# Optimization experiments

Hardware: AMD Instinct MI355X
Metric: run time of the kernel (lower is better)

The kernel has to match this reference:

```python
import jax, jax.numpy as jnp
import numpy as np

BETA = 0.95
THR = 1.0
NUM_STEPS = 100
ALPHA = 2.0  # snntorch atan surrogate default

@jax.custom_vjp
def atan_spike(x):
    return (x > 0).astype(x.dtype)

def _as_fwd(x):
    return (x > 0).astype(x.dtype), x

def _as_bwd(x, g):
    return (g * (ALPHA / 2) / (1 + (jnp.pi / 2 * ALPHA * x) ** 2),)

atan_spike.defvjp(_as_fwd, _as_bwd)


def setup_inputs() -> dict:
    key = jax.random.key(0)
    ks = jax.random.split(key, 9)
    B = 16384
    SH, NH, CO, OUT = 1024, 1024, 256, 64
    s = 0.05
    return {
        "x": jax.random.normal(ks[0], (B, 105), jnp.float32),
        "snn_w1": jax.random.normal(ks[1], (SH, 5), jnp.float32) * s,
        "snn_b1": jnp.zeros((SH,), jnp.float32),
        "snn_w2": jax.random.normal(ks[2], (OUT, SH), jnp.float32) * s,
        "snn_b2": jnp.zeros((OUT,), jnp.float32),
        "nn_w1": jax.random.normal(ks[3], (NH, 5), jnp.float32) * s,
        "nn_b1": jnp.zeros((NH,), jnp.float32),
        "nn_w2": jax.random.normal(ks[4], (OUT, NH), jnp.float32) * s,
        "nn_b2": jnp.zeros((OUT,), jnp.float32),
        "conv_w": jax.random.normal(ks[5], (32, 1, 3), jnp.float32) * s,
        "conv_b": jnp.zeros((32,), jnp.float32),
        "cnn_fc_w": jax.random.normal(ks[6], (CO, 32 * 50), jnp.float32) * s,
        "cnn_fc_b": jnp.zeros((CO,), jnp.float32),
        "comb_w": jax.random.normal(ks[7], (OUT, 2 * OUT + CO), jnp.float32) * s,
        "comb_b": jnp.zeros((OUT,), jnp.float32),
    }


def _forward(x, snn_w1, snn_b1, snn_w2, snn_b2, nn_w1, nn_b1, nn_w2, nn_b2,
             conv_w, conv_b, cnn_fc_w, cnn_fc_b, comb_w, comb_b):
    feats = x[:, :5]                 # [B,5]
    wave = x[:, 5:][:, None, :]      # [B,1,100]
    B = x.shape[0]

    # ---- SNN branch (LIF, beta leak, subtract reset, threshold 1.0) ----
    cur1 = feats @ snn_w1.T + snn_b1  # input current is constant across steps

    def step(carry, _):
        mem1, spk1, mem2, spk2 = carry
        # reset term uses detached spike (snntorch mem_reset detaches)
        mem1 = BETA * mem1 + cur1 - jax.lax.stop_gradient(spk1) * THR
        spk1 = atan_spike(mem1 - THR)
        cur2 = spk1 @ snn_w2.T + snn_b2
        mem2 = BETA * mem2 + cur2 - jax.lax.stop_gradient(spk2) * THR
        spk2 = atan_spike(mem2 - THR)
        return (mem1, spk1, mem2, spk2), spk2

    z1 = jnp.zeros_like(cur1)
    z2 = jnp.zeros((B, snn_w2.shape[0]), cur1.dtype)
    _, spk_rec = jax.lax.scan(step, (z1, z1, z2, z2), None, length=NUM_STEPS)
    snn_out = spk_rec.mean(axis=0)   # [B,OUT]

    # ---- MLP branch ----
    nn_out = jax.nn.relu(feats @ nn_w1.T + nn_b1) @ nn_w2.T + nn_b2

    # ---- CNN branch ----
    c = jax.lax.conv_general_dilated(wave, conv_w, (1,), [(1, 1)],
                                     dimension_numbers=("NCW", "OIW", "NCW"))
    c = jax.nn.relu(c + conv_b[None, :, None])   # [B,32,100]
    c = c.reshape(B, 32, 50, 2).max(axis=-1)      # MaxPool1d(k=2,s=2)
    cnn_out = c.reshape(B, -1) @ cnn_fc_w.T + cnn_fc_b

    combined = jnp.concatenate([snn_out, nn_out, cnn_out], axis=1)
    return combined @ comb_w.T + comb_b


def reference(x, snn_w1, snn_b1, snn_w2, snn_b2, nn_w1, nn_b1, nn_w2, nn_b2,
              conv_w, conv_b, cnn_fc_w, cnn_fc_b, comb_w, comb_b):
    return _forward(x, snn_w1, snn_b1, snn_w2, snn_b2, nn_w1, nn_b1, nn_w2,
                    nn_b2, conv_w, conv_b, cnn_fc_w, cnn_fc_b, comb_w, comb_b)
```

## Files before the change

### kernel.cpp

```cpp
#include <hip/hip_runtime.h>

typedef __bf16 bf16x8_t __attribute__((ext_vector_type(8)));
typedef float f32x4_t __attribute__((ext_vector_type(4)));
typedef float f32x2_t __attribute__((ext_vector_type(2)));

#define NSTEPS 100
#define PB0 0u
#define PB1 32768u
#define COMBF 51200u

static __device__ __forceinline__ unsigned short f2bfu(float v) {
  union { __bf16 h; unsigned short u; } c; c.h = (__bf16)v; return c.u;
}
static __device__ __forceinline__ unsigned int pack2bf(float a, float b) {
  return (unsigned)f2bfu(a) | ((unsigned)f2bfu(b) << 16);
}
static __device__ __forceinline__ float asf(unsigned u) {
  union { unsigned u; float f; } c; c.u = u; return c.f;
}
static __device__ __forceinline__ unsigned asu(float f) {
  union { float f; unsigned u; } c; c.f = f; return c.u;
}
union BF8U { unsigned int u[4]; bf16x8_t v; };

static __device__ __forceinline__ bf16x8_t bfrag_f32(const float* __restrict__ p, float s) {
  BF8U r;
#pragma unroll
  for (int i = 0; i < 4; ++i) r.u[i] = pack2bf(p[2*i]*s, p[2*i+1]*s);
  return r.v;
}

static __device__ __forceinline__ void comb_store(unsigned char* ldsp, int k, int row, float v) {
  *(unsigned short*)(ldsp + COMBF +
      (unsigned)((k >> 5)*1024 + (((k >> 3) & 3)*16 + row)*16 + (k & 7)*2)) = f2bfu(v);
}

__global__ __launch_bounds__(512, 2)
void hybrid_v5(const float* __restrict__ x,
               const float* __restrict__ snn_w1, const float* __restrict__ snn_b1,
               const float* __restrict__ snn_w2, const float* __restrict__ snn_b2,
               const float* __restrict__ nn_w1,  const float* __restrict__ nn_b1,
               const float* __restrict__ nn_w2,  const float* __restrict__ nn_b2,
               const float* __restrict__ conv_w, const float* __restrict__ conv_b,
               const float* __restrict__ fc_w,   const float* __restrict__ fc_b,
               const float* __restrict__ comb_w, const float* __restrict__ comb_b,
               const unsigned short* __restrict__ fcwb, int use_bf,
               float* __restrict__ out)
{
  __shared__ __align__(16) unsigned char lds[65536];
  const int tid  = threadIdx.x;
  const int w    = tid >> 6;
  const int l    = tid & 63;
  const int q    = l >> 4;
  const int m    = l & 15;
  const int row0 = blockIdx.x * 16;

  const int hi  = w >> 2;
  const int ntr = w & 3;
  const int rn  = ntr*16 + m;
  const int rA  = hi*4 + q;
  const int rB  = rA + 8;

  const float* xr = x + (row0 + m)*105;
  const float f0 = xr[0], f1 = xr[1], f2 = xr[2], f3 = xr[3], f4 = xr[4];
  const float b2l = snn_b2[rn];

  bf16x8_t bfr[4][4];
#pragma unroll
  for (int ci = 0; ci < 4; ++ci)
#pragma unroll
    for (int nt = 0; nt < 4; ++nt)
      bfr[ci][nt] = bfrag_f32(snn_w2 + (nt*16 + m)*1024 + (w*4 + ci)*32 + q*8, 1.f);

  f32x2_t cb[16], mb[16];
  {
    const int kb = w*128 + q*8;
#pragma unroll
    for (int ci = 0; ci < 4; ++ci) {
      const float* wp = snn_w1 + (kb + ci*32)*5;
      float wa[40];
#pragma unroll
      for (int u2 = 0; u2 < 10; ++u2) {
        const float4 t4 = *(const float4*)(wp + u2*4);
        wa[u2*4+0] = t4.x; wa[u2*4+1] = t4.y; wa[u2*4+2] = t4.z; wa[u2*4+3] = t4.w;
      }
      float cc[8];
#pragma unroll
      for (int j = 0; j < 8; ++j)
        cc[j] = f0*wa[j*5] + f1*wa[j*5+1] + f2*wa[j*5+2] + f3*wa[j*5+3] + f4*wa[j*5+4]
              + snn_b1[kb + ci*32 + j];
#pragma unroll
      for (int jj = 0; jj < 4; ++jj) {
        cb[ci*4+jj].x = cc[2*jj];   cb[ci*4+jj].y = cc[2*jj+1];
        mb[ci*4+jj].x = 0.f;        mb[ci*4+jj].y = 0.f;
      }
    }
  }

  BF8U afr[4];
#pragma unroll
  for (int ci = 0; ci < 4; ++ci)
#pragma unroll
    for (int jj = 0; jj < 4; ++jj) afr[ci].u[jj] = 0u;

  auto lif_step = [&]() {
#pragma clang fp contract(off)
#pragma unroll
    for (int ci = 0; ci < 4; ++ci) {
#pragma unroll
      for (int jj = 0; jj < 4; ++jj) {
        const int idx = ci*4 + jj;
        const unsigned u = afr[ci].u[jj];
        f32x2_t sp;
        sp.x = asf(u << 16);
        sp.y = asf(u & 0xFFFF0000u);
        f32x2_t mm = mb[idx];
        mm = mm * 0.95f;
        mm = mm + cb[idx];
        mm = mm - sp;
        mb[idx] = mm;
        const float t0 = mm.x > 1.f ? 1.f : 0.f;
        const float t1 = mm.y > 1.f ? 1.f : 0.f;
        afr[ci].u[jj] = __builtin_amdgcn_perm(asu(t1), asu(t0), 0x07060302u);
      }
    }
  };
  lif_step();

  float m2A = 0.f, s2A = 0.f, cntA = 0.f;
  float m2B = 0.f, s2B = 0.f, cntB = 0.f;

  const unsigned pbase  = (unsigned)(ntr*1024 + hi*256 + m*16 + q*4);
  const unsigned wtbase = (unsigned)((w*4*64 + l)*16);
  const f32x4_t z4 = {0.f, 0.f, 0.f, 0.f};

  auto phase = [&](unsigned cur, unsigned prv, bool doRead, bool doLif) {
    float vA[8], vB[8];
    if (doRead) {
#pragma unroll
      for (int s = 0; s < 8; ++s) vA[s] = *(const float*)(lds + prv + pbase + (unsigned)(s*4096));
#pragma unroll
      for (int s = 0; s < 8; ++s) vB[s] = *(const float*)(lds + prv + pbase + 512u + (unsigned)(s*4096));
    }
    f32x4_t acc[4] = {z4, z4, z4, z4};
#pragma unroll
    for (int ci = 0; ci < 4; ++ci)
#pragma unroll
      for (int nt = 0; nt < 4; ++nt)
        acc[nt] = __builtin_amdgcn_mfma_f32_16x16x32_bf16(afr[ci].v, bfr[ci][nt], acc[nt], 0,0,0);
#pragma unroll
    for (int nt = 0; nt < 4; ++nt)
      *(f32x4_t*)(lds + cur + wtbase + (unsigned)(nt*1024)) = acc[nt];
    if (doLif) lif_step();
    if (doRead) {
      float curA = (((vA[0]+vA[1]) + (vA[2]+vA[3])) + ((vA[4]+vA[5]) + (vA[6]+vA[7]))) + b2l;
      float curB = (((vB[0]+vB[1]) + (vB[2]+vB[3])) + ((vB[4]+vB[5]) + (vB[6]+vB[7]))) + b2l;
      m2A = __fsub_rn(__fadd_rn(__fmul_rn(0.95f, m2A), curA), s2A);
      s2A = m2A > 1.f ? 1.f : 0.f;  cntA += s2A;
      m2B = __fsub_rn(__fadd_rn(__fmul_rn(0.95f, m2B), curB), s2B);
      s2B = m2B > 1.f ? 1.f : 0.f;  cntB += s2B;
    }
    __syncthreads();
  };

#pragma unroll 1
  for (int tt = 0; tt < NSTEPS; tt += 2) {
    phase(PB0, PB1, tt > 0, true);
    phase(PB1, PB0, true,  tt + 1 < NSTEPS - 1);
  }

#pragma unroll
  for (int ci = 0; ci < 4; ++ci)
#pragma unroll
    for (int nt = 0; nt < 4; ++nt)
      bfr[ci][nt] = bfrag_f32(nn_w2 + (nt*16 + m)*1024 + (w*4 + ci)*32 + q*8, 1.f);
  {
    float vA[8], vB[8];
#pragma unroll
    for (int s = 0; s < 8; ++s) vA[s] = *(const float*)(lds + PB1 + pbase + (unsigned)(s*4096));
#pragma unroll
    for (int s = 0; s < 8; ++s) vB[s] = *(const float*)(lds + PB1 + pbase + 512u + (unsigned)(s*4096));
    float curA = (((vA[0]+vA[1]) + (vA[2]+vA[3])) + ((vA[4]+vA[5]) + (vA[6]+vA[7]))) + b2l;
    float curB = (((vB[0]+vB[1]) + (vB[2]+vB[3])) + ((vB[4]+vB[5]) + (vB[6]+vB[7]))) + b2l;
    m2A = __fsub_rn(__fadd_rn(__fmul_rn(0.95f, m2A), curA), s2A);
    s2A = m2A > 1.f ? 1.f : 0.f;  cntA += s2A;
    m2B = __fsub_rn(__fadd_rn(__fmul_rn(0.95f, m2B), curB), s2B);
    s2B = m2B > 1.f ? 1.f : 0.f;  cntB += s2B;

    BF8U hfr[4];
    const int kb = w*128 + q*8;
#pragma unroll
    for (int ci = 0; ci < 4; ++ci) {
      const float* wp = nn_w1 + (kb + ci*32)*5;
      float wa[40];
#pragma unroll
      for (int u2 = 0; u2 < 10; ++u2) {
        const float4 t4 = *(const float4*)(wp + u2*4);
        wa[u2*4+0] = t4.x; wa[u2*4+1] = t4.y; wa[u2*4+2] = t4.z; wa[u2*4+3] = t4.w;
      }
      float hv[8];
#pragma unroll
      for (int j = 0; j < 8; ++j) {
        const float h = f0*wa[j*5] + f1*wa[j*5+1] + f2*wa[j*5+2] + f3*wa[j*5+3] + f4*wa[j*5+4]
                      + nn_b1[kb + ci*32 + j];
        hv[j] = fmaxf(h, 0.f);
      }
#pragma unroll
      for (int jj = 0; jj < 4; ++jj) hfr[ci].u[jj] = pack2bf(hv[2*jj], hv[2*jj+1]);
    }
    f32x4_t acc[4] = {z4, z4, z4, z4};
#pragma unroll
    for (int ci = 0; ci < 4; ++ci)
#pragma unroll
      for (int nt = 0; nt < 4; ++nt)
        acc[nt] = __builtin_amdgcn_mfma_f32_16x16x32_bf16(hfr[ci].v, bfr[ci][nt], acc[nt], 0,0,0);
#pragma unroll
    for (int nt = 0; nt < 4; ++nt)
      *(f32x4_t*)(lds + PB0 + wtbase + (unsigned)(nt*1024)) = acc[nt];
  }
  __syncthreads();
  {
    float vA[8], vB[8];
#pragma unroll
    for (int s = 0; s < 8; ++s) vA[s] = *(const float*)(lds + PB0 + pbase + (unsigned)(s*4096));
#pragma unroll
    for (int s = 0; s < 8; ++s) vB[s] = *(const float*)(lds + PB0 + pbase + 512u + (unsigned)(s*4096));
    const float nA = (((vA[0]+vA[1]) + (vA[2]+vA[3])) + ((vA[4]+vA[5]) + (vA[6]+vA[7]))) + nn_b2[rn];
    const float nB = (((vB[0]+vB[1]) + (vB[2]+vB[3])) + ((vB[4]+vB[5]) + (vB[6]+vB[7]))) + nn_b2[rn];
    comb_store(lds, rn,      rA, cntA * 0.0078125f);
    comb_store(lds, rn,      rB, cntB * 0.0078125f);
    comb_store(lds, 64 + rn, rA, nA);
    comb_store(lds, 64 + rn, rB, nB);
  }
  __syncthreads();

  {
    const int ch = tid >> 4;
    const float cw0 = conv_w[ch*3+0], cw1 = conv_w[ch*3+1], cw2 = conv_w[ch*3+2];
    const float cbb = conv_b[ch];
    const float* xw = xr + 5;
    float xm1 = 0.f, x0v = xw[0];
#pragma unroll 1
    for (int p = 0; p < 50; ++p) {
      const float xp1 = xw[2*p + 1];
      const float xp2 = (p < 49) ? xw[2*p + 2] : 0.f;
      const float av = cw0*xm1 + cw1*x0v + cw2*xp1 + cbb;
      const float bv = cw0*x0v + cw1*xp1 + cw2*xp2 + cbb;
      const float pv = fmaxf(fmaxf(av, 0.f), fmaxf(bv, 0.f));
      const int k = ch*50 + p;
      *(unsigned short*)(lds + (unsigned)((k>>5)*1024 + (((k>>3)&3)*16 + m)*16 + (k&7)*2)) = f2bfu(pv);
      xm1 = xp1; x0v = xp2;
    }
  }
  __syncthreads();

  {
    const int c0 = (w*2 + 0)*16 + m;
    const int c1 = (w*2 + 1)*16 + m;
    f32x4_t e0 = z4, o0 = z4, e1 = z4, o1 = z4;
    if (use_bf) {
#pragma unroll 2
      for (int kc = 0; kc < 50; kc += 2) {
        const bf16x8_t a0 = *(const bf16x8_t*)(lds + (unsigned)((kc*64 + l)*16));
        const bf16x8_t a1 = *(const bf16x8_t*)(lds + (unsigned)(((kc+1)*64 + l)*16));
        e0 = __builtin_amdgcn_mfma_f32_16x16x32_bf16(a0, *(const bf16x8_t*)(fcwb + c0*1600 + kc*32 + q*8), e0, 0,0,0);
        o0 = __builtin_amdgcn_mfma_f32_16x16x32_bf16(a1, *(const bf16x8_t*)(fcwb + c0*1600 + (kc+1)*32 + q*8), o0, 0,0,0);
        e1 = __builtin_amdgcn_mfma_f32_16x16x32_bf16(a0, *(const bf16x8_t*)(fcwb + c1*1600 + kc*32 + q*8), e1, 0,0,0);
        o1 = __builtin_amdgcn_mfma_f32_16x16x32_bf16(a1, *(const bf16x8_t*)(fcwb + c1*1600 + (kc+1)*32 + q*8), o1, 0,0,0);
      }
    } else {
#pragma unroll 2
      for (int kc = 0; kc < 50; kc += 2) {
        const bf16x8_t a0 = *(const bf16x8_t*)(lds + (unsigned)((kc*64 + l)*16));
        const bf16x8_t a1 = *(const bf16x8_t*)(lds + (unsigned)(((kc+1)*64 + l)*16));
        e0 = __builtin_amdgcn_mfma_f32_16x16x32_bf16(a0, bfrag_f32(fc_w + c0*1600 + kc*32 + q*8, 1.f), e0, 0,0,0);
        o0 = __builtin_amdgcn_mfma_f32_16x16x32_bf16(a1, bfrag_f32(fc_w + c0*1600 + (kc+1)*32 + q*8, 1.f), o0, 0,0,0);
        e1 = __builtin_amdgcn_mfma_f32_16x16x32_bf16(a0, bfrag_f32(fc_w + c1*1600 + kc*32 + q*8, 1.f), e1, 0,0,0);
        o1 = __builtin_amdgcn_mfma_f32_16x16x32_bf16(a1, bfrag_f32(fc_w + c1*1600 + (kc+1)*32 + q*8, 1.f), o1, 0,0,0);
      }
    }
    const float fb0 = fc_b[c0], fb1 = fc_b[c1];
#pragma unroll
    for (int r = 0; r < 4; ++r) {
      comb_store(lds, 128 + c0, q*4 + r, (e0[r] + o0[r]) + fb0);
      comb_store(lds, 128 + c1, q*4 + r, (e1[r] + o1[r]) + fb1);
    }
  }
  __syncthreads();

  if (w < 4) {
    const int cn = w*16 + m;
    f32x4_t oe = z4, oo = z4;
#pragma unroll
    for (int kc = 0; kc < 12; kc += 2) {
      const bf16x8_t a0 = *(const bf16x8_t*)(lds + COMBF + (unsigned)((kc*64 + l)*16));
      const bf16x8_t a1 = *(const bf16x8_t*)(lds + COMBF + (unsigned)(((kc+1)*64 + l)*16));
      const float s0 = (kc    < 2) ? 1.28f : 1.f;
      const float s1 = (kc+1 < 2) ? 1.28f : 1.f;
      oe = __builtin_amdgcn_mfma_f32_16x16x32_bf16(a0, bfrag_f32(comb_w + cn*384 + kc*32 + q*8, s0), oe, 0,0,0);
      oo = __builtin_amdgcn_mfma_f32_16x16x32_bf16(a1, bfrag_f32(comb_w + cn*384 + (kc+1)*32 + q*8, s1), oo, 0,0,0);
    }
    const float cb2 = comb_b[cn];
#pragma unroll
    for (int r = 0; r < 4; ++r)
      out[(row0 + q*4 + r)*64 + cn] = (oe[r] + oo[r]) + cb2;
  }
}

__global__ __launch_bounds__(256)
void fcw_to_bf16(const float* __restrict__ src, unsigned short* __restrict__ dst) {
  const int i = (blockIdx.x * 256 + threadIdx.x) * 4;
  const float4 v = *(const float4*)(src + i);
  ushort4 o;
  o.x = f2bfu(v.x); o.y = f2bfu(v.y); o.z = f2bfu(v.z); o.w = f2bfu(v.w);
  *(ushort4*)(dst + i) = o;
}

extern "C" void kernel_launch(void* const* d_in, const int* in_sizes, int n_in,
                              void* d_out, int out_size, void* d_ws, size_t ws_size,
                              hipStream_t stream) {
  const float* x       = (const float*)d_in[0];
  const float* snn_w1  = (const float*)d_in[1];
  const float* snn_b1  = (const float*)d_in[2];
  const float* snn_w2  = (const float*)d_in[3];
  const float* snn_b2  = (const float*)d_in[4];
  const float* nn_w1   = (const float*)d_in[5];
  const float* nn_b1   = (const float*)d_in[6];
  const float* nn_w2   = (const float*)d_in[7];
  const float* nn_b2   = (const float*)d_in[8];
  const float* conv_w  = (const float*)d_in[9];
  const float* conv_b  = (const float*)d_in[10];
  const float* fc_w    = (const float*)d_in[11];
  const float* fc_b    = (const float*)d_in[12];
  const float* comb_w  = (const float*)d_in[13];
  const float* comb_b  = (const float*)d_in[14];
  float* outp = (float*)d_out;

  const int rows = in_sizes[0] / 105;
  const int grid = rows / 16;

  const size_t fcw_elems = (size_t)in_sizes[11];
  const int use_bf = (ws_size >= fcw_elems * 2) ? 1 : 0;
  unsigned short* fcwb = (unsigned short*)d_ws;
  if (use_bf) {
    fcw_to_bf16<<<dim3((unsigned)(fcw_elems / 1024)), dim3(256), 0, stream>>>(fc_w, fcwb);
  }

  hybrid_v5<<<dim3(grid), dim3(512), 0, stream>>>(
      x, snn_w1, snn_b1, snn_w2, snn_b2,
      nn_w1, nn_b1, nn_w2, nn_b2,
      conv_w, conv_b, fc_w, fc_b, comb_w, comb_b,
      fcwb, use_bf, outp);
}
```

Measured before the change: 766.5 us.

## Halve block to four waves with wider per-wave K slice in SNN loop

Launches 256-thread blocks instead of 512, giving each wave twice as many hidden neurons (8 K-chunks) in the recurrent SNN step and the MLP/CNN stages. This cuts the cross-wave LDS partial-sum reduction from 8 to 4 partials per step and makes the barrier cover fewer waves. In exchange, per-wave register use roughly doubles (weights and membrane state held in VGPRs) and fewer waves are resident to hide latency, while each wave issues twice as many serial MFMAs per step. The LIF update also switches from packed float2 math to scalar rn intrinsics.

Result: slower. 820.0 us (+7.0%).

```diff
diff --git a/kernel.cpp b/kernel.cpp
--- a/kernel.cpp
+++ b/kernel.cpp
@@ -2,11 +2,10 @@
 
 typedef __bf16 bf16x8_t __attribute__((ext_vector_type(8)));
 typedef float f32x4_t __attribute__((ext_vector_type(4)));
-typedef float f32x2_t __attribute__((ext_vector_type(2)));
 
 #define NSTEPS 100
 #define PB0 0u
-#define PB1 32768u
+#define PB1 16384u
 #define COMBF 51200u
 
 static __device__ __forceinline__ unsigned short f2bfu(float v) {
@@ -35,8 +34,8 @@
       (unsigned)((k >> 5)*1024 + (((k >> 3) & 3)*16 + row)*16 + (k & 7)*2)) = f2bfu(v);
 }
 
-__global__ __launch_bounds__(512, 2)
-void hybrid_v5(const float* __restrict__ x,
+__global__ __launch_bounds__(256, 1)
+void hybrid_v8(const float* __restrict__ x,
                const float* __restrict__ snn_w1, const float* __restrict__ snn_b1,
                const float* __restrict__ snn_w2, const float* __restrict__ snn_b2,
                const float* __restrict__ nn_w1,  const float* __restrict__ nn_b1,
@@ -55,28 +54,24 @@
   const int m    = l & 15;
   const int row0 = blockIdx.x * 16;
 
-  const int hi  = w >> 2;
-  const int ntr = w & 3;
-  const int rn  = ntr*16 + m;
-  const int rA  = hi*4 + q;
-  const int rB  = rA + 8;
+  const int rcol = w*16 + m;
 
   const float* xr = x + (row0 + m)*105;
   const float f0 = xr[0], f1 = xr[1], f2 = xr[2], f3 = xr[3], f4 = xr[4];
-  const float b2l = snn_b2[rn];
-
-  bf16x8_t bfr[4][4];
-#pragma unroll
-  for (int ci = 0; ci < 4; ++ci)
+  const float b2l = snn_b2[rcol];
+
+  bf16x8_t bfr[8][4];
+#pragma unroll
+  for (int ci = 0; ci < 8; ++ci)
 #pragma unroll
     for (int nt = 0; nt < 4; ++nt)
-      bfr[ci][nt] = bfrag_f32(snn_w2 + (nt*16 + m)*1024 + (w*4 + ci)*32 + q*8, 1.f);
-
-  f32x2_t cb[16], mb[16];
-  {
-    const int kb = w*128 + q*8;
-#pragma unroll
-    for (int ci = 0; ci < 4; ++ci) {
+      bfr[ci][nt] = bfrag_f32(snn_w2 + (nt*16 + m)*1024 + (w*8 + ci)*32 + q*8, 1.f);
+
+  float c[64], mem[64];
+  {
+    const int kb = w*256 + q*8;
+#pragma unroll
+    for (int ci = 0; ci < 8; ++ci) {
       const float* wp = snn_w1 + (kb + ci*32)*5;
       float wa[40];
 #pragma unroll
@@ -84,67 +79,58 @@
         const float4 t4 = *(const float4*)(wp + u2*4);
         wa[u2*4+0] = t4.x; wa[u2*4+1] = t4.y; wa[u2*4+2] = t4.z; wa[u2*4+3] = t4.w;
       }
-      float cc[8];
-#pragma unroll
-      for (int j = 0; j < 8; ++j)
-        cc[j] = f0*wa[j*5] + f1*wa[j*5+1] + f2*wa[j*5+2] + f3*wa[j*5+3] + f4*wa[j*5+4]
-              + snn_b1[kb + ci*32 + j];
+#pragma unroll
+      for (int j = 0; j < 8; ++j) {
+        c[ci*8+j] = f0*wa[j*5] + f1*wa[j*5+1] + f2*wa[j*5+2] + f3*wa[j*5+3] + f4*wa[j*5+4]
+                  + snn_b1[kb + ci*32 + j];
+        mem[ci*8+j] = 0.f;
+      }
+    }
+  }
+
+  BF8U afr[8];
+#pragma unroll
+  for (int ci = 0; ci < 8; ++ci)
+#pragma unroll
+    for (int jj = 0; jj < 4; ++jj) afr[ci].u[jj] = 0u;
+
+  auto lif_step = [&]() {
+#pragma unroll
+    for (int ci = 0; ci < 8; ++ci) {
 #pragma unroll
       for (int jj = 0; jj < 4; ++jj) {
-        cb[ci*4+jj].x = cc[2*jj];   cb[ci*4+jj].y = cc[2*jj+1];
-        mb[ci*4+jj].x = 0.f;        mb[ci*4+jj].y = 0.f;
-      }
-    }
-  }
-
-  BF8U afr[4];
-#pragma unroll
-  for (int ci = 0; ci < 4; ++ci)
-#pragma unroll
-    for (int jj = 0; jj < 4; ++jj) afr[ci].u[jj] = 0u;
-
-  auto lif_step = [&]() {
-#pragma clang fp contract(off)
-#pragma unroll
-    for (int ci = 0; ci < 4; ++ci) {
-#pragma unroll
-      for (int jj = 0; jj < 4; ++jj) {
-        const int idx = ci*4 + jj;
+        const int i0 = ci*8 + 2*jj;
         const unsigned u = afr[ci].u[jj];
-        f32x2_t sp;
-        sp.x = asf(u << 16);
-        sp.y = asf(u & 0xFFFF0000u);
-        f32x2_t mm = mb[idx];
-        mm = mm * 0.95f;
-        mm = mm + cb[idx];
-        mm = mm - sp;
-        mb[idx] = mm;
-        const float t0 = mm.x > 1.f ? 1.f : 0.f;
-        const float t1 = mm.y > 1.f ? 1.f : 0.f;
+        const float sp0 = asf(u << 16);
+        const float sp1 = asf(u & 0xFFFF0000u);
+        mem[i0]   = __fsub_rn(__fadd_rn(__fmul_rn(0.95f, mem[i0]),   c[i0]),   sp0);
+        mem[i0+1] = __fsub_rn(__fadd_rn(__fmul_rn(0.95f, mem[i0+1]), c[i0+1]), sp1);
+        const float t0 = mem[i0]   > 1.f ? 1.f : 0.f;
+        const float t1 = mem[i0+1] > 1.f ? 1.f : 0.f;
         afr[ci].u[jj] = __builtin_amdgcn_perm(asu(t1), asu(t0), 0x07060302u);
       }
     }
   };
   lif_step();
 
-  float m2A = 0.f, s2A = 0.f, cntA = 0.f;
-  float m2B = 0.f, s2B = 0.f, cntB = 0.f;
-
-  const unsigned pbase  = (unsigned)(ntr*1024 + hi*256 + m*16 + q*4);
-  const unsigned wtbase = (unsigned)((w*4*64 + l)*16);
+  float m2[4] = {0.f,0.f,0.f,0.f}, s2[4] = {0.f,0.f,0.f,0.f}, cnt[4] = {0.f,0.f,0.f,0.f};
+
+  const unsigned wtbase = (unsigned)(w*4096 + l*16);
+  const unsigned rbase  = (unsigned)(w*1024 + (l&15)*16 + (l>>4)*4);
   const f32x4_t z4 = {0.f, 0.f, 0.f, 0.f};
 
   auto phase = [&](unsigned cur, unsigned prv, bool doRead, bool doLif) {
-    float vA[8], vB[8];
+    float v[16];
     if (doRead) {
 #pragma unroll
-      for (int s = 0; s < 8; ++s) vA[s] = *(const float*)(lds + prv + pbase + (unsigned)(s*4096));
-#pragma unroll
-      for (int s = 0; s < 8; ++s) vB[s] = *(const float*)(lds + prv + pbase + 512u + (unsigned)(s*4096));
+      for (int s = 0; s < 4; ++s)
+#pragma unroll
+        for (int i = 0; i < 4; ++i)
+          v[s*4+i] = *(const float*)(lds + prv + rbase + (unsigned)(s*4096 + i*256));
     }
     f32x4_t acc[4] = {z4, z4, z4, z4};
 #pragma unroll
-    for (int ci = 0; ci < 4; ++ci)
+    for (int ci = 0; ci < 8; ++ci)
 #pragma unroll
       for (int nt = 0; nt < 4; ++nt)
         acc[nt] = __builtin_amdgcn_mfma_f32_16x16x32_bf16(afr[ci].v, bfr[ci][nt], acc[nt], 0,0,0);
@@ -153,12 +139,12 @@
       *(f32x4_t*)(lds + cur + wtbase + (unsigned)(nt*1024)) = acc[nt];
     if (doLif) lif_step();
     if (doRead) {
-      float curA = (((vA[0]+vA[1]) + (vA[2]+vA[3])) + ((vA[4]+vA[5]) + (vA[6]+vA[7]))) + b2l;
-      float curB = (((vB[0]+vB[1]) + (vB[2]+vB[3])) + ((vB[4]+vB[5]) + (vB[6]+vB[7]))) + b2l;
-      m2A = __fsub_rn(__fadd_rn(__fmul_rn(0.95f, m2A), curA), s2A);
-      s2A = m2A > 1.f ? 1.f : 0.f;  cntA += s2A;
-      m2B = __fsub_rn(__fadd_rn(__fmul_rn(0.95f, m2B), curB), s2B);
-      s2B = m2B > 1.f ? 1.f : 0.f;  cntB += s2B;
+#pragma unroll
+      for (int i = 0; i < 4; ++i) {
+        const float cc = ((v[0+i] + v[4+i]) + (v[8+i] + v[12+i])) + b2l;
+        m2[i] = __fsub_rn(__fadd_rn(__fmul_rn(0.95f, m2[i]), cc), s2[i]);
+        s2[i] = m2[i] > 1.f ? 1.f : 0.f;  cnt[i] += s2[i];
+      }
     }
     __syncthreads();
   };
@@ -170,27 +156,28 @@
   }
 
 #pragma unroll
-  for (int ci = 0; ci < 4; ++ci)
+  for (int ci = 0; ci < 8; ++ci)
 #pragma unroll
     for (int nt = 0; nt < 4; ++nt)
-      bfr[ci][nt] = bfrag_f32(nn_w2 + (nt*16 + m)*1024 + (w*4 + ci)*32 + q*8, 1.f);
-  {
-    float vA[8], vB[8];
-#pragma unroll
-    for (int s = 0; s < 8; ++s) vA[s] = *(const float*)(lds + PB1 + pbase + (unsigned)(s*4096));
-#pragma unroll
-    for (int s = 0; s < 8; ++s) vB[s] = *(const float*)(lds + PB1 + pbase + 512u + (unsigned)(s*4096));
-    float curA = (((vA[0]+vA[1]) + (vA[2]+vA[3])) + ((vA[4]+vA[5]) + (vA[6]+vA[7]))) + b2l;
-    float curB = (((vB[0]+vB[1]) + (vB[2]+vB[3])) + ((vB[4]+vB[5]) + (vB[6]+vB[7]))) + b2l;
-    m2A = __fsub_rn(__fadd_rn(__fmul_rn(0.95f, m2A), curA), s2A);
-    s2A = m2A > 1.f ? 1.f : 0.f;  cntA += s2A;
-    m2B = __fsub_rn(__fadd_rn(__fmul_rn(0.95f, m2B), curB), s2B);
-    s2B = m2B > 1.f ? 1.f : 0.f;  cntB += s2B;
-
-    BF8U hfr[4];
-    const int kb = w*128 + q*8;
-#pragma unroll
-    for (int ci = 0; ci < 4; ++ci) {
+      bfr[ci][nt] = bfrag_f32(nn_w2 + (nt*16 + m)*1024 + (w*8 + ci)*32 + q*8, 1.f);
+  {
+    float v[16];
+#pragma unroll
+    for (int s = 0; s < 4; ++s)
+#pragma unroll
+      for (int i = 0; i < 4; ++i)
+        v[s*4+i] = *(const float*)(lds + PB1 + rbase + (unsigned)(s*4096 + i*256));
+#pragma unroll
+    for (int i = 0; i < 4; ++i) {
+      const float cc = ((v[0+i] + v[4+i]) + (v[8+i] + v[12+i])) + b2l;
+      m2[i] = __fsub_rn(__fadd_rn(__fmul_rn(0.95f, m2[i]), cc), s2[i]);
+      s2[i] = m2[i] > 1.f ? 1.f : 0.f;  cnt[i] += s2[i];
+    }
+
+    BF8U hfr[8];
+    const int kb = w*256 + q*8;
+#pragma unroll
+    for (int ci = 0; ci < 8; ++ci) {
       const float* wp = nn_w1 + (kb + ci*32)*5;
       float wa[40];
 #pragma unroll
@@ -210,7 +197,7 @@
     }
     f32x4_t acc[4] = {z4, z4, z4, z4};
 #pragma unroll
-    for (int ci = 0; ci < 4; ++ci)
+    for (int ci = 0; ci < 8; ++ci)
 #pragma unroll
       for (int nt = 0; nt < 4; ++nt)
         acc[nt] = __builtin_amdgcn_mfma_f32_16x16x32_bf16(hfr[ci].v, bfr[ci][nt], acc[nt], 0,0,0);
@@ -220,75 +207,87 @@
   }
   __syncthreads();
   {
-    float vA[8], vB[8];
-#pragma unroll
-    for (int s = 0; s < 8; ++s) vA[s] = *(const float*)(lds + PB0 + pbase + (unsigned)(s*4096));
-#pragma unroll
-    for (int s = 0; s < 8; ++s) vB[s] = *(const float*)(lds + PB0 + pbase + 512u + (unsigned)(s*4096));
-    const float nA = (((vA[0]+vA[1]) + (vA[2]+vA[3])) + ((vA[4]+vA[5]) + (vA[6]+vA[7]))) + nn_b2[rn];
-    const float nB = (((vB[0]+vB[1]) + (vB[2]+vB[3])) + ((vB[4]+vB[5]) + (vB[6]+vB[7]))) + nn_b2[rn];
-    comb_store(lds, rn,      rA, cntA * 0.0078125f);
-    comb_store(lds, rn,      rB, cntB * 0.0078125f);
-    comb_store(lds, 64 + rn, rA, nA);
-    comb_store(lds, 64 + rn, rB, nB);
+    float v[16];
+#pragma unroll
+    for (int s = 0; s < 4; ++s)
+#pragma unroll
+      for (int i = 0; i < 4; ++i)
+        v[s*4+i] = *(const float*)(lds + PB0 + rbase + (unsigned)(s*4096 + i*256));
+#pragma unroll
+    for (int i = 0; i < 4; ++i) {
+      const float nv = ((v[0+i] + v[4+i]) + (v[8+i] + v[12+i])) + nn_b2[rcol];
+      comb_store(lds, rcol,      i*4 + q, cnt[i] * 0.0078125f);
+      comb_store(lds, 64 + rcol, i*4 + q, nv);
+    }
   }
   __syncthreads();
 
   {
     const int ch = tid >> 4;
-    const float cw0 = conv_w[ch*3+0], cw1 = conv_w[ch*3+1], cw2 = conv_w[ch*3+2];
-    const float cbb = conv_b[ch];
+    const float a0w = conv_w[ch*3+0], a1w = conv_w[ch*3+1], a2w = conv_w[ch*3+2];
+    const float b0w = conv_w[(ch+16)*3+0], b1w = conv_w[(ch+16)*3+1], b2w = conv_w[(ch+16)*3+2];
+    const float cba = conv_b[ch], cbb = conv_b[ch+16];
     const float* xw = xr + 5;
     float xm1 = 0.f, x0v = xw[0];
 #pragma unroll 1
     for (int p = 0; p < 50; ++p) {
       const float xp1 = xw[2*p + 1];
       const float xp2 = (p < 49) ? xw[2*p + 2] : 0.f;
-      const float av = cw0*xm1 + cw1*x0v + cw2*xp1 + cbb;
-      const float bv = cw0*x0v + cw1*xp1 + cw2*xp2 + cbb;
-      const float pv = fmaxf(fmaxf(av, 0.f), fmaxf(bv, 0.f));
-      const int k = ch*50 + p;
-      *(unsigned short*)(lds + (unsigned)((k>>5)*1024 + (((k>>3)&3)*16 + m)*16 + (k&7)*2)) = f2bfu(pv);
+      const float aa = a0w*xm1 + a1w*x0v + a2w*xp1 + cba;
+      const float ab = a0w*x0v + a1w*xp1 + a2w*xp2 + cba;
+      const float pa = fmaxf(fmaxf(aa, 0.f), fmaxf(ab, 0.f));
+      const float ba = b0w*xm1 + b1w*x0v + b2w*xp1 + cbb;
+      const float bb = b0w*x0v + b1w*xp1 + b2w*xp2 + cbb;
+      const float pb = fmaxf(fmaxf(ba, 0.f), fmaxf(bb, 0.f));
+      const int ka = ch*50 + p;
+      const int kb2 = (ch+16)*50 + p;
+      *(unsigned short*)(lds + (unsigned)((ka>>5)*1024 + (((ka>>3)&3)*16 + m)*16 + (ka&7)*2)) = f2bfu(pa);
+      *(unsigned short*)(lds + (unsigned)((kb2>>5)*1024 + (((kb2>>3)&3)*16 + m)*16 + (kb2&7)*2)) = f2bfu(pb);
       xm1 = xp1; x0v = xp2;
     }
   }
   __syncthreads();
 
   {
-    const int c0 = (w*2 + 0)*16 + m;
-    const int c1 = (w*2 + 1)*16 + m;
-    f32x4_t e0 = z4, o0 = z4, e1 = z4, o1 = z4;
+    f32x4_t fe[4] = {z4, z4, z4, z4};
+    f32x4_t fo[4] = {z4, z4, z4, z4};
     if (use_bf) {
 #pragma unroll 2
       for (int kc = 0; kc < 50; kc += 2) {
         const bf16x8_t a0 = *(const bf16x8_t*)(lds + (unsigned)((kc*64 + l)*16));
         const bf16x8_t a1 = *(const bf16x8_t*)(lds + (unsigned)(((kc+1)*64 + l)*16));
-        e0 = __builtin_amdgcn_mfma_f32_16x16x32_bf16(a0, *(const bf16x8_t*)(fcwb + c0*1600 + kc*32 + q*8), e0, 0,0,0);
-        o0 = __builtin_amdgcn_mfma_f32_16x16x32_bf16(a1, *(const bf16x8_t*)(fcwb + c0*1600 + (kc+1)*32 + q*8), o0, 0,0,0);
-        e1 = __builtin_amdgcn_mfma_f32_16x16x32_bf16(a0, *(const bf16x8_t*)(fcwb + c1*1600 + kc*32 + q*8), e1, 0,0,0);
-        o1 = __builtin_amdgcn_mfma_f32_16x16x32_bf16(a1, *(const bf16x8_t*)(fcwb + c1*1600 + (kc+1)*32 + q*8), o1, 0,0,0);
+#pragma unroll
+        for (int nt = 0; nt < 4; ++nt) {
+          const int cn = w*64 + nt*16 + m;
+          fe[nt] = __builtin_amdgcn_mfma_f32_16x16x32_bf16(a0, *(const bf16x8_t*)(fcwb + cn*1600 + kc*32 + q*8), fe[nt], 0,0,0);
+          fo[nt] = __builtin_amdgcn_mfma_f32_16x16x32_bf16(a1, *(const bf16x8_t*)(fcwb + cn*1600 + (kc+1)*32 + q*8), fo[nt], 0,0,0);
+        }
       }
     } else {
 #pragma unroll 2
       for (int kc = 0; kc < 50; kc += 2) {
         const bf16x8_t a0 = *(const bf16x8_t*)(lds + (unsigned)((kc*64 + l)*16));
         const bf16x8_t a1 = *(const bf16x8_t*)(lds + (unsigned)(((kc+1)*64 + l)*16));
-        e0 = __builtin_amdgcn_mfma_f32_16x16x32_bf16(a0, bfrag_f32(fc_w + c0*1600 + kc*32 + q*8, 1.f), e0, 0,0,0);
-        o0 = __builtin_amdgcn_mfma_f32_16x16x32_bf16(a1, bfrag_f32(fc_w + c0*1600 + (kc+1)*32 + q*8, 1.f), o0, 0,0,0);
-        e1 = __builtin_amdgcn_mfma_f32_16x16x32_bf16(a0, bfrag_f32(fc_w + c1*1600 + kc*32 + q*8, 1.f), e1, 0,0,0);
-        o1 = __builtin_amdgcn_mfma_f32_16x16x32_bf16(a1, bfrag_f32(fc_w + c1*1600 + (kc+1)*32 + q*8, 1.f), o1, 0,0,0);
-      }
-    }
-    const float fb0 = fc_b[c0], fb1 = fc_b[c1];
-#pragma unroll
-    for (int r = 0; r < 4; ++r) {
-      comb_store(lds, 128 + c0, q*4 + r, (e0[r] + o0[r]) + fb0);
-      comb_store(lds, 128 + c1, q*4 + r, (e1[r] + o1[r]) + fb1);
+#pragma unroll
+        for (int nt = 0; nt < 4; ++nt) {
+          const int cn = w*64 + nt*16 + m;
+          fe[nt] = __builtin_amdgcn_mfma_f32_16x16x32_bf16(a0, bfrag_f32(fc_w + cn*1600 + kc*32 + q*8, 1.f), fe[nt], 0,0,0);
+          fo[nt] = __builtin_amdgcn_mfma_f32_16x16x32_bf16(a1, bfrag_f32(fc_w + cn*1600 + (kc+1)*32 + q*8, 1.f), fo[nt], 0,0,0);
+        }
+      }
+    }
+#pragma unroll
+    for (int nt = 0; nt < 4; ++nt) {
+      const int cn = w*64 + nt*16 + m;
+      const float fb = fc_b[cn];
+#pragma unroll
+      for (int r = 0; r < 4; ++r)
+        comb_store(lds, 128 + cn, q*4 + r, (fe[nt][r] + fo[nt][r]) + fb);
     }
   }
   __syncthreads();
 
-  if (w < 4) {
+  {
     const int cn = w*16 + m;
     f32x4_t oe = z4, oo = z4;
 #pragma unroll
@@ -346,7 +345,7 @@
     fcw_to_bf16<<<dim3((unsigned)(fcw_elems / 1024)), dim3(256), 0, stream>>>(fc_w, fcwb);
   }
 
-  hybrid_v5<<<dim3(grid), dim3(512), 0, stream>>>(
+  hybrid_v8<<<dim3(grid), dim3(256), 0, stream>>>(
       x, snn_w1, snn_b1, snn_w2, snn_b2,
       nn_w1, nn_b1, nn_w2, nn_b2,
       conv_w, conv_b, fc_w, fc_b, comb_w, comb_b,
```

## Specialize warps into LIF producers and MFMA consumers with LDS spike exchange

Applied to the files above, without the earlier changes.

Splits the 8 waves into two roles. Four waves run the layer-1 LIF update over 256 neurons each and write bf16 spike fragments to double-buffered LDS. The other four waves hold the snn_w2 fragments for their K slice, run the MFMAs, reduce partial sums through LDS and update the layer-2 LIF. The goal is to overlap the elementwise LIF work with the matrix work across steps and to cut the per-wave partial-sum reduction from 8 ways to 4. The cost is higher register use per wave, since each producer wave keeps 32 state pairs and each consumer wave keeps 32 weight fragments. LDS grows to 96 KB of dynamic shared memory, which may lower occupancy below the 2 blocks per CU requested in launch_bounds.

Measured after the change: 779.7 us. Within noise of the previous version (+1.7%).

```diff
diff --git a/kernel.cpp b/kernel.cpp
--- a/kernel.cpp
+++ b/kernel.cpp
@@ -5,9 +5,11 @@
 typedef float f32x2_t __attribute__((ext_vector_type(2)));
 
 #define NSTEPS 100
-#define PB0 0u
-#define PB1 32768u
-#define COMBF 51200u
+#define SB0 0u
+#define SB1 32768u
+#define PBU0 65536u
+#define PBU1 81920u
+#define COMBF 86016u
 
 static __device__ __forceinline__ unsigned short f2bfu(float v) {
   union { __bf16 h; unsigned short u; } c; c.h = (__bf16)v; return c.u;
@@ -36,7 +38,7 @@
 }
 
 __global__ __launch_bounds__(512, 2)
-void hybrid_v5(const float* __restrict__ x,
+void hybrid_v9(const float* __restrict__ x,
                const float* __restrict__ snn_w1, const float* __restrict__ snn_b1,
                const float* __restrict__ snn_w2, const float* __restrict__ snn_b2,
                const float* __restrict__ nn_w1,  const float* __restrict__ nn_b1,
@@ -47,7 +49,7 @@
                const unsigned short* __restrict__ fcwb, int use_bf,
                float* __restrict__ out)
 {
-  __shared__ __align__(16) unsigned char lds[65536];
+  extern __shared__ __align__(16) unsigned char lds[];
   const int tid  = threadIdx.x;
   const int w    = tid >> 6;
   const int l    = tid & 63;
@@ -55,28 +57,15 @@
   const int m    = l & 15;
   const int row0 = blockIdx.x * 16;
 
-  const int hi  = w >> 2;
-  const int ntr = w & 3;
-  const int rn  = ntr*16 + m;
-  const int rA  = hi*4 + q;
-  const int rB  = rA + 8;
-
   const float* xr = x + (row0 + m)*105;
   const float f0 = xr[0], f1 = xr[1], f2 = xr[2], f3 = xr[3], f4 = xr[4];
-  const float b2l = snn_b2[rn];
-
-  bf16x8_t bfr[4][4];
-#pragma unroll
-  for (int ci = 0; ci < 4; ++ci)
-#pragma unroll
-    for (int nt = 0; nt < 4; ++nt)
-      bfr[ci][nt] = bfrag_f32(snn_w2 + (nt*16 + m)*1024 + (w*4 + ci)*32 + q*8, 1.f);
-
-  f32x2_t cb[16], mb[16];
-  {
-    const int kb = w*128 + q*8;
-#pragma unroll
-    for (int ci = 0; ci < 4; ++ci) {
+  const f32x4_t z4 = {0.f, 0.f, 0.f, 0.f};
+
+  if (w < 4) {
+    f32x2_t cb[32], mb[32];
+    const int kb = w*256 + q*8;
+#pragma unroll
+    for (int ci = 0; ci < 8; ++ci) {
       const float* wp = snn_w1 + (kb + ci*32)*5;
       float wa[40];
 #pragma unroll
@@ -91,148 +80,178 @@
               + snn_b1[kb + ci*32 + j];
 #pragma unroll
       for (int jj = 0; jj < 4; ++jj) {
-        cb[ci*4+jj].x = cc[2*jj];   cb[ci*4+jj].y = cc[2*jj+1];
-        mb[ci*4+jj].x = 0.f;        mb[ci*4+jj].y = 0.f;
-      }
-    }
-  }
-
-  BF8U afr[4];
-#pragma unroll
-  for (int ci = 0; ci < 4; ++ci)
-#pragma unroll
-    for (int jj = 0; jj < 4; ++jj) afr[ci].u[jj] = 0u;
-
-  auto lif_step = [&]() {
+        cb[ci*4+jj].x = cc[2*jj];  cb[ci*4+jj].y = cc[2*jj+1];
+        mb[ci*4+jj].x = 0.f;       mb[ci*4+jj].y = 0.f;
+      }
+    }
+    BF8U afr[8];
+#pragma unroll
+    for (int ci = 0; ci < 8; ++ci)
+#pragma unroll
+      for (int jj = 0; jj < 4; ++jj) afr[ci].u[jj] = 0u;
+
+    auto lif_step = [&]() {
 #pragma clang fp contract(off)
 #pragma unroll
-    for (int ci = 0; ci < 4; ++ci) {
-#pragma unroll
-      for (int jj = 0; jj < 4; ++jj) {
-        const int idx = ci*4 + jj;
-        const unsigned u = afr[ci].u[jj];
-        f32x2_t sp;
-        sp.x = asf(u << 16);
-        sp.y = asf(u & 0xFFFF0000u);
-        f32x2_t mm = mb[idx];
-        mm = mm * 0.95f;
-        mm = mm + cb[idx];
-        mm = mm - sp;
-        mb[idx] = mm;
-        const float t0 = mm.x > 1.f ? 1.f : 0.f;
-        const float t1 = mm.y > 1.f ? 1.f : 0.f;
-        afr[ci].u[jj] = __builtin_amdgcn_perm(asu(t1), asu(t0), 0x07060302u);
-      }
-    }
-  };
-  lif_step();
-
-  float m2A = 0.f, s2A = 0.f, cntA = 0.f;
-  float m2B = 0.f, s2B = 0.f, cntB = 0.f;
-
-  const unsigned pbase  = (unsigned)(ntr*1024 + hi*256 + m*16 + q*4);
-  const unsigned wtbase = (unsigned)((w*4*64 + l)*16);
-  const f32x4_t z4 = {0.f, 0.f, 0.f, 0.f};
-
-  auto phase = [&](unsigned cur, unsigned prv, bool doRead, bool doLif) {
-    float vA[8], vB[8];
-    if (doRead) {
-#pragma unroll
-      for (int s = 0; s < 8; ++s) vA[s] = *(const float*)(lds + prv + pbase + (unsigned)(s*4096));
-#pragma unroll
-      for (int s = 0; s < 8; ++s) vB[s] = *(const float*)(lds + prv + pbase + 512u + (unsigned)(s*4096));
-    }
-    f32x4_t acc[4] = {z4, z4, z4, z4};
-#pragma unroll
-    for (int ci = 0; ci < 4; ++ci)
+      for (int ci = 0; ci < 8; ++ci) {
+#pragma unroll
+        for (int jj = 0; jj < 4; ++jj) {
+          const int idx = ci*4 + jj;
+          const unsigned u = afr[ci].u[jj];
+          f32x2_t sp;
+          sp.x = asf(u << 16);
+          sp.y = asf(u & 0xFFFF0000u);
+          f32x2_t mm = mb[idx];
+          mm = mm * 0.95f;
+          mm = mm + cb[idx];
+          mm = mm - sp;
+          mb[idx] = mm;
+          const float t0 = mm.x > 1.f ? 1.f : 0.f;
+          const float t1 = mm.y > 1.f ? 1.f : 0.f;
+          afr[ci].u[jj] = __builtin_amdgcn_perm(asu(t1), asu(t0), 0x07060302u);
+        }
+      }
+    };
+    lif_step();
+#pragma unroll
+    for (int ci = 0; ci < 8; ++ci)
+      *(bf16x8_t*)(lds + SB0 + (unsigned)(((w*8 + ci)*64 + l)*16)) = afr[ci].v;
+    __syncthreads();
+
+#pragma unroll 1
+    for (int t = 0; t < NSTEPS; ++t) {
+      if (t < NSTEPS - 1) {
+        lif_step();
+        const unsigned sb = ((t + 1) & 1) ? SB1 : SB0;
+#pragma unroll
+        for (int ci = 0; ci < 8; ++ci)
+          *(bf16x8_t*)(lds + sb + (unsigned)(((w*8 + ci)*64 + l)*16)) = afr[ci].v;
+      }
+      __syncthreads();
+    }
+
+    {
+      BF8U hfr[8];
+#pragma unroll
+      for (int ci = 0; ci < 8; ++ci) {
+        const float* wp = nn_w1 + (kb + ci*32)*5;
+        float wa[40];
+#pragma unroll
+        for (int u2 = 0; u2 < 10; ++u2) {
+          const float4 t4 = *(const float4*)(wp + u2*4);
+          wa[u2*4+0] = t4.x; wa[u2*4+1] = t4.y; wa[u2*4+2] = t4.z; wa[u2*4+3] = t4.w;
+        }
+        float hv[8];
+#pragma unroll
+        for (int j = 0; j < 8; ++j) {
+          const float h = f0*wa[j*5] + f1*wa[j*5+1] + f2*wa[j*5+2] + f3*wa[j*5+3] + f4*wa[j*5+4]
+                        + nn_b1[kb + ci*32 + j];
+          hv[j] = fmaxf(h, 0.f);
+        }
+#pragma unroll
+        for (int jj = 0; jj < 4; ++jj) hfr[ci].u[jj] = pack2bf(hv[2*jj], hv[2*jj+1]);
+      }
+#pragma unroll
+      for (int ci = 0; ci < 8; ++ci)
+        *(bf16x8_t*)(lds + SB0 + (unsigned)(((w*8 + ci)*64 + l)*16)) = hfr[ci].v;
+    }
+    __syncthreads();
+    __syncthreads();
+  } else {
+    const int wm  = w - 4;
+    const int col = wm*16 + m;
+    const float b2l = snn_b2[col];
+
+    bf16x8_t bfr[8][4];
+#pragma unroll
+    for (int ci = 0; ci < 8; ++ci)
 #pragma unroll
       for (int nt = 0; nt < 4; ++nt)
-        acc[nt] = __builtin_amdgcn_mfma_f32_16x16x32_bf16(afr[ci].v, bfr[ci][nt], acc[nt], 0,0,0);
-#pragma unroll
-    for (int nt = 0; nt < 4; ++nt)
-      *(f32x4_t*)(lds + cur + wtbase + (unsigned)(nt*1024)) = acc[nt];
-    if (doLif) lif_step();
-    if (doRead) {
-      float curA = (((vA[0]+vA[1]) + (vA[2]+vA[3])) + ((vA[4]+vA[5]) + (vA[6]+vA[7]))) + b2l;
-      float curB = (((vB[0]+vB[1]) + (vB[2]+vB[3])) + ((vB[4]+vB[5]) + (vB[6]+vB[7]))) + b2l;
-      m2A = __fsub_rn(__fadd_rn(__fmul_rn(0.95f, m2A), curA), s2A);
-      s2A = m2A > 1.f ? 1.f : 0.f;  cntA += s2A;
-      m2B = __fsub_rn(__fadd_rn(__fmul_rn(0.95f, m2B), curB), s2B);
-      s2B = m2B > 1.f ? 1.f : 0.f;  cntB += s2B;
-    }
-    __syncthreads();
-  };
+        bfr[ci][nt] = bfrag_f32(snn_w2 + (nt*16 + m)*1024 + (wm*8 + ci)*32 + q*8, 1.f);
+
+    float m2[4] = {0.f,0.f,0.f,0.f}, s2[4] = {0.f,0.f,0.f,0.f}, cnt[4] = {0.f,0.f,0.f,0.f};
+    __syncthreads();
 
 #pragma unroll 1
-  for (int tt = 0; tt < NSTEPS; tt += 2) {
-    phase(PB0, PB1, tt > 0, true);
-    phase(PB1, PB0, true,  tt + 1 < NSTEPS - 1);
-  }
-
-#pragma unroll
-  for (int ci = 0; ci < 4; ++ci)
-#pragma unroll
-    for (int nt = 0; nt < 4; ++nt)
-      bfr[ci][nt] = bfrag_f32(nn_w2 + (nt*16 + m)*1024 + (w*4 + ci)*32 + q*8, 1.f);
-  {
-    float vA[8], vB[8];
-#pragma unroll
-    for (int s = 0; s < 8; ++s) vA[s] = *(const float*)(lds + PB1 + pbase + (unsigned)(s*4096));
-#pragma unroll
-    for (int s = 0; s < 8; ++s) vB[s] = *(const float*)(lds + PB1 + pbase + 512u + (unsigned)(s*4096));
-    float curA = (((vA[0]+vA[1]) + (vA[2]+vA[3])) + ((vA[4]+vA[5]) + (vA[6]+vA[7]))) + b2l;
-    float curB = (((vB[0]+vB[1]) + (vB[2]+vB[3])) + ((vB[4]+vB[5]) + (vB[6]+vB[7]))) + b2l;
-    m2A = __fsub_rn(__fadd_rn(__fmul_rn(0.95f, m2A), curA), s2A);
-    s2A = m2A > 1.f ? 1.f : 0.f;  cntA += s2A;
-    m2B = __fsub_rn(__fadd_rn(__fmul_rn(0.95f, m2B), curB), s2B);
-    s2B = m2B > 1.f ? 1.f : 0.f;  cntB += s2B;
-
-    BF8U hfr[4];
-    const int kb = w*128 + q*8;
-#pragma unroll
-    for (int ci = 0; ci < 4; ++ci) {
-      const float* wp = nn_w1 + (kb + ci*32)*5;
-      float wa[40];
-#pragma unroll
-      for (int u2 = 0; u2 < 10; ++u2) {
-        const float4 t4 = *(const float4*)(wp + u2*4);
-        wa[u2*4+0] = t4.x; wa[u2*4+1] = t4.y; wa[u2*4+2] = t4.z; wa[u2*4+3] = t4.w;
-      }
-      float hv[8];
-#pragma unroll
-      for (int j = 0; j < 8; ++j) {
-        const float h = f0*wa[j*5] + f1*wa[j*5+1] + f2*wa[j*5+2] + f3*wa[j*5+3] + f4*wa[j*5+4]
-                      + nn_b1[kb + ci*32 + j];
-        hv[j] = fmaxf(h, 0.f);
-      }
-#pragma unroll
-      for (int jj = 0; jj < 4; ++jj) hfr[ci].u[jj] = pack2bf(hv[2*jj], hv[2*jj+1]);
-    }
-    f32x4_t acc[4] = {z4, z4, z4, z4};
-#pragma unroll
-    for (int ci = 0; ci < 4; ++ci)
+    for (int t = 0; t < NSTEPS; ++t) {
+      const unsigned sb = (t & 1) ? SB1 : SB0;
+      const unsigned pc = (t & 1) ? PBU1 : PBU0;
+      const unsigned pp = (t & 1) ? PBU0 : PBU1;
+      f32x4_t p0, p1, p2, p3;
+      if (t > 0) {
+        p0 = *(const f32x4_t*)(lds + pp + (unsigned)(((0*4 + wm)*64 + l)*16));
+        p1 = *(const f32x4_t*)(lds + pp + (unsigned)(((1*4 + wm)*64 + l)*16));
+        p2 = *(const f32x4_t*)(lds + pp + (unsigned)(((2*4 + wm)*64 + l)*16));
+        p3 = *(const f32x4_t*)(lds + pp + (unsigned)(((3*4 + wm)*64 + l)*16));
+      }
+      f32x4_t acc[4] = {z4, z4, z4, z4};
+#pragma unroll
+      for (int ci = 0; ci < 8; ++ci) {
+        const bf16x8_t a = *(const bf16x8_t*)(lds + sb + (unsigned)(((wm*8 + ci)*64 + l)*16));
+#pragma unroll
+        for (int nt = 0; nt < 4; ++nt)
+          acc[nt] = __builtin_amdgcn_mfma_f32_16x16x32_bf16(a, bfr[ci][nt], acc[nt], 0,0,0);
+      }
 #pragma unroll
       for (int nt = 0; nt < 4; ++nt)
-        acc[nt] = __builtin_amdgcn_mfma_f32_16x16x32_bf16(hfr[ci].v, bfr[ci][nt], acc[nt], 0,0,0);
-#pragma unroll
-    for (int nt = 0; nt < 4; ++nt)
-      *(f32x4_t*)(lds + PB0 + wtbase + (unsigned)(nt*1024)) = acc[nt];
-  }
-  __syncthreads();
-  {
-    float vA[8], vB[8];
-#pragma unroll
-    for (int s = 0; s < 8; ++s) vA[s] = *(const float*)(lds + PB0 + pbase + (unsigned)(s*4096));
-#pragma unroll
-    for (int s = 0; s < 8; ++s) vB[s] = *(const float*)(lds + PB0 + pbase + 512u + (unsigned)(s*4096));
-    const float nA = (((vA[0]+vA[1]) + (vA[2]+vA[3])) + ((vA[4]+vA[5]) + (vA[6]+vA[7]))) + nn_b2[rn];
-    const float nB = (((vB[0]+vB[1]) + (vB[2]+vB[3])) + ((vB[4]+vB[5]) + (vB[6]+vB[7]))) + nn_b2[rn];
-    comb_store(lds, rn,      rA, cntA * 0.0078125f);
-    comb_store(lds, rn,      rB, cntB * 0.0078125f);
-    comb_store(lds, 64 + rn, rA, nA);
-    comb_store(lds, 64 + rn, rB, nB);
-  }
-  __syncthreads();
+        *(f32x4_t*)(lds + pc + (unsigned)(((wm*4 + nt)*64 + l)*16)) = acc[nt];
+      if (t > 0) {
+#pragma unroll
+        for (int r = 0; r < 4; ++r) {
+          const float cc = ((p0[r] + p1[r]) + (p2[r] + p3[r])) + b2l;
+          m2[r] = __fsub_rn(__fadd_rn(__fmul_rn(0.95f, m2[r]), cc), s2[r]);
+          s2[r] = m2[r] > 1.f ? 1.f : 0.f;  cnt[r] += s2[r];
+        }
+      }
+      __syncthreads();
+    }
+
+    {
+      const f32x4_t p0 = *(const f32x4_t*)(lds + PBU1 + (unsigned)(((0*4 + wm)*64 + l)*16));
+      const f32x4_t p1 = *(const f32x4_t*)(lds + PBU1 + (unsigned)(((1*4 + wm)*64 + l)*16));
+      const f32x4_t p2 = *(const f32x4_t*)(lds + PBU1 + (unsigned)(((2*4 + wm)*64 + l)*16));
+      const f32x4_t p3 = *(const f32x4_t*)(lds + PBU1 + (unsigned)(((3*4 + wm)*64 + l)*16));
+#pragma unroll
+      for (int r = 0; r < 4; ++r) {
+        const float cc = ((p0[r] + p1[r]) + (p2[r] + p3[r])) + b2l;
+        m2[r] = __fsub_rn(__fadd_rn(__fmul_rn(0.95f, m2[r]), cc), s2[r]);
+        s2[r] = m2[r] > 1.f ? 1.f : 0.f;  cnt[r] += s2[r];
+      }
+#pragma unroll
+      for (int ci = 0; ci < 8; ++ci)
+#pragma unroll
+        for (int nt = 0; nt < 4; ++nt)
+          bfr[ci][nt] = bfrag_f32(nn_w2 + (nt*16 + m)*1024 + (wm*8 + ci)*32 + q*8, 1.f);
+    }
+    __syncthreads();
+    {
+      f32x4_t acc[4] = {z4, z4, z4, z4};
+#pragma unroll
+      for (int ci = 0; ci < 8; ++ci) {
+        const bf16x8_t a = *(const bf16x8_t*)(lds + SB0 + (unsigned)(((wm*8 + ci)*64 + l)*16));
+#pragma unroll
+        for (int nt = 0; nt < 4; ++nt)
+          acc[nt] = __builtin_amdgcn_mfma_f32_16x16x32_bf16(a, bfr[ci][nt], acc[nt], 0,0,0);
+      }
+#pragma unroll
+      for (int nt = 0; nt < 4; ++nt)
+        *(f32x4_t*)(lds + PBU0 + (unsigned)(((wm*4 + nt)*64 + l)*16)) = acc[nt];
+    }
+    __syncthreads();
+    {
+      const f32x4_t p0 = *(const f32x4_t*)(lds + PBU0 + (unsigned)(((0*4 + wm)*64 + l)*16));
+      const f32x4_t p1 = *(const f32x4_t*)(lds + PBU0 + (unsigned)(((1*4 + wm)*64 + l)*16));
+      const f32x4_t p2 = *(const f32x4_t*)(lds + PBU0 + (unsigned)(((2*4 + wm)*64 + l)*16));
+      const f32x4_t p3 = *(const f32x4_t*)(lds + PBU0 + (unsigned)(((3*4 + wm)*64 + l)*16));
+      const float nnb = nn_b2[col];
+#pragma unroll
+      for (int r = 0; r < 4; ++r) {
+        const float nv = ((p0[r] + p1[r]) + (p2[r] + p3[r])) + nnb;
+        comb_store(lds, col,      q*4 + r, cnt[r] * 0.0078125f);
+        comb_store(lds, 64 + col, q*4 + r, nv);
+      }
+    }
+  }
 
   {
     const int ch = tid >> 4;
@@ -339,6 +358,9 @@
   const int rows = in_sizes[0] / 105;
   const int grid = rows / 16;
 
+  (void)hipFuncSetAttribute((const void*)hybrid_v9,
+                            hipFuncAttributeMaxDynamicSharedMemorySize, 98304);
+
   const size_t fcw_elems = (size_t)in_sizes[11];
   const int use_bf = (ws_size >= fcw_elems * 2) ? 1 : 0;
   unsigned short* fcwb = (unsigned short*)d_ws;
@@ -346,7 +368,7 @@
     fcw_to_bf16<<<dim3((unsigned)(fcw_elems / 1024)), dim3(256), 0, stream>>>(fc_w, fcwb);
   }
 
-  hybrid_v5<<<dim3(grid), dim3(512), 0, stream>>>(
+  hybrid_v9<<<dim3(grid), dim3(512), 98304, stream>>>(
       x, snn_w1, snn_b1, snn_w2, snn_b2,
       nn_w1, nn_b1, nn_w2, nn_b2,
       conv_w, conv_b, fc_w, fc_b, comb_w, comb_b,
```
